# Optimization experiments

Hardware: AMD Instinct MI355X
Metric: run time of the kernel (lower is better)

Reference implementation:

```python
import jax, jax.numpy as jnp
import numpy as np

WORKSPACE_RADIUS = 1.0
WORKSPACE_HEIGHT = 1.0


def setup_inputs() -> dict:
    key = jax.random.key(0)
    k1, k2 = jax.random.split(key)
    # (B, N, 6): xyz + normals, already padded to common length N
    pointclouds = jax.random.normal(k1, (32, 131072, 6), dtype=jnp.float32)
    # (B, 4, 4): homogeneous task transforms
    task_transform = jax.random.normal(k2, (32, 4, 4), dtype=jnp.float32)
    return {"pointclouds": pointclouds, "task_transform": task_transform}


def reference(pointclouds, task_transform):
    # Split xyz points and normals
    pts = pointclouds[..., :3]          # (B, N, 3)
    nrm = pointclouds[..., 3:]          # (B, N, 3)

    rot = task_transform[:, :3, :3]     # (B, 3, 3)
    trans = task_transform[:, :3, 3]    # (B, 3)

    # points @ rotation + translation (matches torch.matmul(points, rotation))
    p = jnp.einsum('bnd,bde->bne', pts, rot) + trans[:, None, :]

    # padded rows have all-zero normals
    non_padded = jnp.sum(nrm, axis=-1) != 0

    sq_dist = p[..., 0] ** 2 + p[..., 1] ** 2
    in_range = (sq_dist < WORKSPACE_RADIUS ** 2) & (p[..., 2] < WORKSPACE_HEIGHT)
    valid = in_range & non_padded      # (B, N)

    # Filter-and-repad: compact valid points to the front (stable = order
    # preserving, as in the torch boolean-index version), zero the tail.
    order = jnp.argsort(~valid, axis=1, stable=True)                 # (B, N)
    gathered = jnp.take_along_axis(pointclouds, order[..., None], axis=1)
    mask_sorted = jnp.take_along_axis(valid, order, axis=1)
    return gathered * mask_sorted[..., None].astype(pointclouds.dtype)
```

## Files before the change

kernel.cpp:

```cpp
#include <hip/hip_runtime.h>
#include <cstdint>

namespace {

constexpr int kB   = 32;
constexpr int kN   = 131072;
constexpr int kC   = 6;
constexpr int TPB  = 256;
constexpr int ROWS_PER_BLK = 512;
constexpr int BPB  = kN / ROWS_PER_BLK;
constexpr int NBLK = kB * BPB;
constexpr int WAVES = TPB / 64;

__device__ __forceinline__ int waveSum(int v) {
#pragma unroll
    for (int off = 32; off; off >>= 1) v += __shfl_xor(v, off, 64);
    return v;
}

__global__ __launch_bounds__(TPB) void k_count(const float* __restrict__ pc,
                                               const float* __restrict__ tt,
                                               uint64_t* __restrict__ masks,
                                               int* __restrict__ blkCnt) {
    const int blk  = blockIdx.x;
    const int b    = blk >> 8;
    const int tid  = threadIdx.x;
    const int lane = tid & 63;
    const int wv   = tid >> 6;

    const float* T = tt + b * 16;
    const float T0 = T[0], T1 = T[1], T2 = T[2],  T3  = T[3];
    const float T4 = T[4], T5 = T[5], T6 = T[6],  T7  = T[7];
    const float T8 = T[8], T9 = T[9], T10 = T[10], T11 = T[11];

    const float4* f4 = (const float4*)pc + (size_t)blk * (ROWS_PER_BLK * kC / 4);
    const float4 q0 = f4[3 * tid];
    const float4 q1 = f4[3 * tid + 1];
    const float4 q2 = f4[3 * tid + 2];

    const float ns0 = (q0.w + q1.x) + q1.y;
    const float px0 = q0.x * T0 + q0.y * T4 + q0.z * T8  + T3;
    const float py0 = q0.x * T1 + q0.y * T5 + q0.z * T9  + T7;
    const float pz0 = q0.x * T2 + q0.y * T6 + q0.z * T10 + T11;
    const bool v0 = (px0 * px0 + py0 * py0 < 1.0f) && (pz0 < 1.0f) && (ns0 != 0.0f);

    const float ns1 = (q2.y + q2.z) + q2.w;
    const float px1 = q1.z * T0 + q1.w * T4 + q2.x * T8  + T3;
    const float py1 = q1.z * T1 + q1.w * T5 + q2.x * T9  + T7;
    const float pz1 = q1.z * T2 + q1.w * T6 + q2.x * T10 + T11;
    const bool v1 = (px1 * px1 + py1 * py1 < 1.0f) && (pz1 < 1.0f) && (ns1 != 0.0f);

    const uint64_t m0 = __ballot(v0);
    const uint64_t m1 = __ballot(v1);

    __shared__ uint64_t sm[WAVES * 2];
    if (lane == 0) {
        sm[wv * 2]     = m0;
        sm[wv * 2 + 1] = m1;
        masks[(size_t)blk * 8 + wv * 2]     = m0;
        masks[(size_t)blk * 8 + wv * 2 + 1] = m1;
    }
    __syncthreads();
    if (wv == 0) {
        int v = (lane < 8) ? __popcll(sm[lane]) : 0;
        v = waveSum(v);
        if (lane == 0) blkCnt[blk] = v;
    }
}

__global__ __launch_bounds__(TPB) void k_scatter(const float* __restrict__ pc,
                                                 const uint64_t* __restrict__ masks,
                                                 const int* __restrict__ blkCnt,
                                                 float* __restrict__ out) {
    const int blk  = blockIdx.x;
    const int b    = blk >> 8;
    const int sub  = blk & (BPB - 1);
    const int tid  = threadIdx.x;
    const int lane = tid & 63;
    const int wv   = tid >> 6;

    __shared__ uint64_t sm[8];
    __shared__ int sRed[2 * WAVES];

    if (tid < 8) sm[tid] = masks[(size_t)blk * 8 + tid];

    const int c = blkCnt[b * BPB + tid];
    const int pw = waveSum((tid < sub) ? c : 0);
    const int tw = waveSum(c);
    if (lane == 0) { sRed[wv] = pw; sRed[WAVES + wv] = tw; }
    __syncthreads();
    const int blockBase = (sRed[0] + sRed[1]) + (sRed[2] + sRed[3]);
    const int total     = (sRed[4] + sRed[5]) + (sRed[6] + sRed[7]);

    const uint64_t m0 = sm[wv * 2], m1 = sm[wv * 2 + 1];
    int wb = 0;
#pragma unroll
    for (int w = 0; w < WAVES - 1; ++w)
        if (w < wv) wb += __popcll(sm[w * 2]) + __popcll(sm[w * 2 + 1]);

    const uint64_t low = (1ull << lane) - 1ull;
    const int beforeE = __popcll(m0 & low) + __popcll(m1 & low);
    const bool v0 = (m0 >> lane) & 1ull;
    const bool v1 = (m1 >> lane) & 1ull;

    const size_t batchF = (size_t)b * kN * kC;
    const int rowBlk = sub * ROWS_PER_BLK + wv * 128 + 2 * lane;
    const int vcnt0 = blockBase + wb + beforeE;
    const int vcnt1 = vcnt0 + (v0 ? 1 : 0);

    if (v0) {
        const float2* r = (const float2*)(pc + batchF + (size_t)rowBlk * kC);
        float2* o = (float2*)(out + batchF + (size_t)vcnt0 * kC);
        o[0] = r[0]; o[1] = r[1]; o[2] = r[2];
    }
    if (v1) {
        const float2* r = (const float2*)(pc + batchF + (size_t)(rowBlk + 1) * kC);
        float2* o = (float2*)(out + batchF + (size_t)vcnt1 * kC);
        o[0] = r[0]; o[1] = r[1]; o[2] = r[2];
    }

    const int tail = kN - total;
    const int len  = (tail + BPB - 1) >> 8;
    const int r0 = total + sub * len;
    const int r1 = min(r0 + len, kN);
    if (r0 < r1) {
        float* base = out + batchF;
        const int f0 = r0 * 6, f1 = r1 * 6;
        if (tid == 0) {
            const float2 zz = make_float2(0.0f, 0.0f);
            if (f0 & 3) *(float2*)(base + f0) = zz;
            if (f1 & 3) *(float2*)(base + (f1 & ~3)) = zz;
        }
        const int a4 = (f0 + 3) >> 2;
        const int b4 = f1 >> 2;
        float4* o4 = (float4*)base;
        const float4 z4 = make_float4(0.0f, 0.0f, 0.0f, 0.0f);
        for (int i = a4 + tid; i < b4; i += TPB) o4[i] = z4;
    }
}

}

extern "C" void kernel_launch(void* const* d_in, const int* in_sizes, int n_in,
                              void* d_out, int out_size, void* d_ws, size_t ws_size,
                              hipStream_t stream) {
    const float* pc = (const float*)d_in[0];
    const float* tt = (const float*)d_in[1];
    float* out = (float*)d_out;

    uint64_t* masks = (uint64_t*)d_ws;
    int* blkCnt     = (int*)((char*)d_ws + (size_t)NBLK * 8 * sizeof(uint64_t));

    k_count<<<NBLK, TPB, 0, stream>>>(pc, tt, masks, blkCnt);
    k_scatter<<<NBLK, TPB, 0, stream>>>(pc, masks, blkCnt, out);
}
```

Measured before the change: 38.95 us.

## Stage block-compacted rows in workspace and emit them with contiguous copies

The first kernel now loads each block's rows coalesced through shared memory, compacts the valid rows within the block, and writes them to a per-block staging buffer in the workspace. The second kernel only copies each block's contiguous valid prefix to its global offset and zero-fills the tail, replacing per-thread scattered reads from the input. This trades sparse, uncoalesced gathers for an extra write and read of the valid data through the workspace, which can add traffic when many points are valid. The old two-kernel path is kept as a fallback when the workspace is too small.

Result: faster. 37.49 us (-3.7%).

```diff
diff --git a/kernel.cpp b/kernel.cpp
--- a/kernel.cpp
+++ b/kernel.cpp
@@ -11,6 +11,7 @@
 constexpr int BPB  = kN / ROWS_PER_BLK;
 constexpr int NBLK = kB * BPB;
 constexpr int WAVES = TPB / 64;
+constexpr int F4_PER_BLK = ROWS_PER_BLK * kC / 4;
 
 __device__ __forceinline__ int waveSum(int v) {
 #pragma unroll
@@ -18,10 +19,11 @@
     return v;
 }
 
-__global__ __launch_bounds__(TPB) void k_count(const float* __restrict__ pc,
-                                               const float* __restrict__ tt,
-                                               uint64_t* __restrict__ masks,
-                                               int* __restrict__ blkCnt) {
+
+__global__ __launch_bounds__(TPB) void k_count_stage(const float* __restrict__ pc,
+                                                     const float* __restrict__ tt,
+                                                     float* __restrict__ staged,
+                                                     int* __restrict__ blkCnt) {
     const int blk  = blockIdx.x;
     const int b    = blk >> 8;
     const int tid  = threadIdx.x;
@@ -33,45 +35,61 @@
     const float T4 = T[4], T5 = T[5], T6 = T[6],  T7  = T[7];
     const float T8 = T[8], T9 = T[9], T10 = T[10], T11 = T[11];
 
-    const float4* f4 = (const float4*)pc + (size_t)blk * (ROWS_PER_BLK * kC / 4);
-    const float4 q0 = f4[3 * tid];
-    const float4 q1 = f4[3 * tid + 1];
-    const float4 q2 = f4[3 * tid + 2];
-
-    const float ns0 = (q0.w + q1.x) + q1.y;
-    const float px0 = q0.x * T0 + q0.y * T4 + q0.z * T8  + T3;
-    const float py0 = q0.x * T1 + q0.y * T5 + q0.z * T9  + T7;
-    const float pz0 = q0.x * T2 + q0.y * T6 + q0.z * T10 + T11;
+    const float4* f4 = (const float4*)pc + (size_t)blk * F4_PER_BLK;
+    const float4 qa = f4[tid];
+    const float4 qb = f4[tid + 256];
+    const float4 qc = f4[tid + 512];
+
+    __shared__ float4 sb[F4_PER_BLK];
+    sb[tid] = qa; sb[tid + 256] = qb; sb[tid + 512] = qc;
+    __syncthreads();
+
+    const float2* s2 = (const float2*)sb;
+    const float2 r0a = s2[6 * tid],     r0b = s2[6 * tid + 1], r0c = s2[6 * tid + 2];
+    const float2 r1a = s2[6 * tid + 3], r1b = s2[6 * tid + 4], r1c = s2[6 * tid + 5];
+
+    const float ns0 = (r0b.y + r0c.x) + r0c.y;
+    const float px0 = r0a.x * T0 + r0a.y * T4 + r0b.x * T8  + T3;
+    const float py0 = r0a.x * T1 + r0a.y * T5 + r0b.x * T9  + T7;
+    const float pz0 = r0a.x * T2 + r0a.y * T6 + r0b.x * T10 + T11;
     const bool v0 = (px0 * px0 + py0 * py0 < 1.0f) && (pz0 < 1.0f) && (ns0 != 0.0f);
 
-    const float ns1 = (q2.y + q2.z) + q2.w;
-    const float px1 = q1.z * T0 + q1.w * T4 + q2.x * T8  + T3;
-    const float py1 = q1.z * T1 + q1.w * T5 + q2.x * T9  + T7;
-    const float pz1 = q1.z * T2 + q1.w * T6 + q2.x * T10 + T11;
+    const float ns1 = (r1b.y + r1c.x) + r1c.y;
+    const float px1 = r1a.x * T0 + r1a.y * T4 + r1b.x * T8  + T3;
+    const float py1 = r1a.x * T1 + r1a.y * T5 + r1b.x * T9  + T7;
+    const float pz1 = r1a.x * T2 + r1a.y * T6 + r1b.x * T10 + T11;
     const bool v1 = (px1 * px1 + py1 * py1 < 1.0f) && (pz1 < 1.0f) && (ns1 != 0.0f);
 
     const uint64_t m0 = __ballot(v0);
     const uint64_t m1 = __ballot(v1);
 
     __shared__ uint64_t sm[WAVES * 2];
-    if (lane == 0) {
-        sm[wv * 2]     = m0;
-        sm[wv * 2 + 1] = m1;
-        masks[(size_t)blk * 8 + wv * 2]     = m0;
-        masks[(size_t)blk * 8 + wv * 2 + 1] = m1;
-    }
-    __syncthreads();
+    if (lane == 0) { sm[wv * 2] = m0; sm[wv * 2 + 1] = m1; }
+    __syncthreads();
+
     if (wv == 0) {
         int v = (lane < 8) ? __popcll(sm[lane]) : 0;
         v = waveSum(v);
         if (lane == 0) blkCnt[blk] = v;
     }
-}
-
-__global__ __launch_bounds__(TPB) void k_scatter(const float* __restrict__ pc,
-                                                 const uint64_t* __restrict__ masks,
-                                                 const int* __restrict__ blkCnt,
-                                                 float* __restrict__ out) {
+
+    int wb = 0;
+#pragma unroll
+    for (int w = 0; w < WAVES - 1; ++w)
+        if (w < wv) wb += __popcll(sm[w * 2]) + __popcll(sm[w * 2 + 1]);
+    const uint64_t low = (1ull << lane) - 1ull;
+    const int beforeE = __popcll(m0 & low) + __popcll(m1 & low);
+    const int rk0 = wb + beforeE;
+    const int rk1 = rk0 + (v0 ? 1 : 0);
+
+    float2* st = (float2*)(staged + (size_t)blk * (ROWS_PER_BLK * kC));
+    if (v0) { float2* o = st + rk0 * 3; o[0] = r0a; o[1] = r0b; o[2] = r0c; }
+    if (v1) { float2* o = st + rk1 * 3; o[0] = r1a; o[1] = r1b; o[2] = r1c; }
+}
+
+__global__ __launch_bounds__(TPB) void k_emit(const float* __restrict__ staged,
+                                              const int* __restrict__ blkCnt,
+                                              float* __restrict__ out) {
     const int blk  = blockIdx.x;
     const int b    = blk >> 8;
     const int sub  = blk & (BPB - 1);
@@ -79,10 +97,7 @@
     const int lane = tid & 63;
     const int wv   = tid >> 6;
 
-    __shared__ uint64_t sm[8];
     __shared__ int sRed[2 * WAVES];
-
-    if (tid < 8) sm[tid] = masks[(size_t)blk * 8 + tid];
 
     const int c = blkCnt[b * BPB + tid];
     const int pw = waveSum((tid < sub) ? c : 0);
@@ -91,33 +106,14 @@
     __syncthreads();
     const int blockBase = (sRed[0] + sRed[1]) + (sRed[2] + sRed[3]);
     const int total     = (sRed[4] + sRed[5]) + (sRed[6] + sRed[7]);
-
-    const uint64_t m0 = sm[wv * 2], m1 = sm[wv * 2 + 1];
-    int wb = 0;
-#pragma unroll
-    for (int w = 0; w < WAVES - 1; ++w)
-        if (w < wv) wb += __popcll(sm[w * 2]) + __popcll(sm[w * 2 + 1]);
-
-    const uint64_t low = (1ull << lane) - 1ull;
-    const int beforeE = __popcll(m0 & low) + __popcll(m1 & low);
-    const bool v0 = (m0 >> lane) & 1ull;
-    const bool v1 = (m1 >> lane) & 1ull;
+    const int myCnt     = blkCnt[blk];
 
     const size_t batchF = (size_t)b * kN * kC;
-    const int rowBlk = sub * ROWS_PER_BLK + wv * 128 + 2 * lane;
-    const int vcnt0 = blockBase + wb + beforeE;
-    const int vcnt1 = vcnt0 + (v0 ? 1 : 0);
-
-    if (v0) {
-        const float2* r = (const float2*)(pc + batchF + (size_t)rowBlk * kC);
-        float2* o = (float2*)(out + batchF + (size_t)vcnt0 * kC);
-        o[0] = r[0]; o[1] = r[1]; o[2] = r[2];
-    }
-    if (v1) {
-        const float2* r = (const float2*)(pc + batchF + (size_t)(rowBlk + 1) * kC);
-        float2* o = (float2*)(out + batchF + (size_t)vcnt1 * kC);
-        o[0] = r[0]; o[1] = r[1]; o[2] = r[2];
-    }
+
+    const float2* src = (const float2*)(staged + (size_t)blk * (ROWS_PER_BLK * kC));
+    float2* dst = (float2*)(out + batchF + (size_t)blockBase * kC);
+    const int nf2 = myCnt * 3;
+    for (int i = tid; i < nf2; i += TPB) dst[i] = src[i];
 
     const int tail = kN - total;
     const int len  = (tail + BPB - 1) >> 8;
@@ -139,6 +135,128 @@
     }
 }
 
+
+__global__ __launch_bounds__(TPB) void k_count(const float* __restrict__ pc,
+                                               const float* __restrict__ tt,
+                                               uint64_t* __restrict__ masks,
+                                               int* __restrict__ blkCnt) {
+    const int blk  = blockIdx.x;
+    const int b    = blk >> 8;
+    const int tid  = threadIdx.x;
+    const int lane = tid & 63;
+    const int wv   = tid >> 6;
+
+    const float* T = tt + b * 16;
+    const float T0 = T[0], T1 = T[1], T2 = T[2],  T3  = T[3];
+    const float T4 = T[4], T5 = T[5], T6 = T[6],  T7  = T[7];
+    const float T8 = T[8], T9 = T[9], T10 = T[10], T11 = T[11];
+
+    const float4* f4 = (const float4*)pc + (size_t)blk * F4_PER_BLK;
+    const float4 q0 = f4[3 * tid];
+    const float4 q1 = f4[3 * tid + 1];
+    const float4 q2 = f4[3 * tid + 2];
+
+    const float ns0 = (q0.w + q1.x) + q1.y;
+    const float px0 = q0.x * T0 + q0.y * T4 + q0.z * T8  + T3;
+    const float py0 = q0.x * T1 + q0.y * T5 + q0.z * T9  + T7;
+    const float pz0 = q0.x * T2 + q0.y * T6 + q0.z * T10 + T11;
+    const bool v0 = (px0 * px0 + py0 * py0 < 1.0f) && (pz0 < 1.0f) && (ns0 != 0.0f);
+
+    const float ns1 = (q2.y + q2.z) + q2.w;
+    const float px1 = q1.z * T0 + q1.w * T4 + q2.x * T8  + T3;
+    const float py1 = q1.z * T1 + q1.w * T5 + q2.x * T9  + T7;
+    const float pz1 = q1.z * T2 + q1.w * T6 + q2.x * T10 + T11;
+    const bool v1 = (px1 * px1 + py1 * py1 < 1.0f) && (pz1 < 1.0f) && (ns1 != 0.0f);
+
+    const uint64_t m0 = __ballot(v0);
+    const uint64_t m1 = __ballot(v1);
+
+    __shared__ uint64_t sm[WAVES * 2];
+    if (lane == 0) {
+        sm[wv * 2]     = m0;
+        sm[wv * 2 + 1] = m1;
+        masks[(size_t)blk * 8 + wv * 2]     = m0;
+        masks[(size_t)blk * 8 + wv * 2 + 1] = m1;
+    }
+    __syncthreads();
+    if (wv == 0) {
+        int v = (lane < 8) ? __popcll(sm[lane]) : 0;
+        v = waveSum(v);
+        if (lane == 0) blkCnt[blk] = v;
+    }
+}
+
+__global__ __launch_bounds__(TPB) void k_scatter(const float* __restrict__ pc,
+                                                 const uint64_t* __restrict__ masks,
+                                                 const int* __restrict__ blkCnt,
+                                                 float* __restrict__ out) {
+    const int blk  = blockIdx.x;
+    const int b    = blk >> 8;
+    const int sub  = blk & (BPB - 1);
+    const int tid  = threadIdx.x;
+    const int lane = tid & 63;
+    const int wv   = tid >> 6;
+
+    __shared__ uint64_t sm[8];
+    __shared__ int sRed[2 * WAVES];
+
+    if (tid < 8) sm[tid] = masks[(size_t)blk * 8 + tid];
+
+    const int c = blkCnt[b * BPB + tid];
+    const int pw = waveSum((tid < sub) ? c : 0);
+    const int tw = waveSum(c);
+    if (lane == 0) { sRed[wv] = pw; sRed[WAVES + wv] = tw; }
+    __syncthreads();
+    const int blockBase = (sRed[0] + sRed[1]) + (sRed[2] + sRed[3]);
+    const int total     = (sRed[4] + sRed[5]) + (sRed[6] + sRed[7]);
+
+    const uint64_t m0 = sm[wv * 2], m1 = sm[wv * 2 + 1];
+    int wb = 0;
+#pragma unroll
+    for (int w = 0; w < WAVES - 1; ++w)
+        if (w < wv) wb += __popcll(sm[w * 2]) + __popcll(sm[w * 2 + 1]);
+
+    const uint64_t low = (1ull << lane) - 1ull;
+    const int beforeE = __popcll(m0 & low) + __popcll(m1 & low);
+    const bool v0 = (m0 >> lane) & 1ull;
+    const bool v1 = (m1 >> lane) & 1ull;
+
+    const size_t batchF = (size_t)b * kN * kC;
+    const int rowBlk = sub * ROWS_PER_BLK + wv * 128 + 2 * lane;
+    const int vcnt0 = blockBase + wb + beforeE;
+    const int vcnt1 = vcnt0 + (v0 ? 1 : 0);
+
+    if (v0) {
+        const float2* r = (const float2*)(pc + batchF + (size_t)rowBlk * kC);
+        float2* o = (float2*)(out + batchF + (size_t)vcnt0 * kC);
+        o[0] = r[0]; o[1] = r[1]; o[2] = r[2];
+    }
+    if (v1) {
+        const float2* r = (const float2*)(pc + batchF + (size_t)(rowBlk + 1) * kC);
+        float2* o = (float2*)(out + batchF + (size_t)vcnt1 * kC);
+        o[0] = r[0]; o[1] = r[1]; o[2] = r[2];
+    }
+
+    const int tail = kN - total;
+    const int len  = (tail + BPB - 1) >> 8;
+    const int r0 = total + sub * len;
+    const int r1 = min(r0 + len, kN);
+    if (r0 < r1) {
+        float* base = out + batchF;
+        const int f0 = r0 * 6, f1 = r1 * 6;
+        if (tid == 0) {
+            const float2 zz = make_float2(0.0f, 0.0f);
+            if (f0 & 3) *(float2*)(base + f0) = zz;
+            if (f1 & 3) *(float2*)(base + (f1 & ~3)) = zz;
+        }
+        const int a4 = (f0 + 3) >> 2;
+        const int b4 = f1 >> 2;
+        float4* o4 = (float4*)base;
+        const float4 z4 = make_float4(0.0f, 0.0f, 0.0f, 0.0f);
+        for (int i = a4 + tid; i < b4; i += TPB) o4[i] = z4;
+    }
+}
+
 }
 
 extern "C" void kernel_launch(void* const* d_in, const int* in_sizes, int n_in,
@@ -148,9 +266,18 @@
     const float* tt = (const float*)d_in[1];
     float* out = (float*)d_out;
 
-    uint64_t* masks = (uint64_t*)d_ws;
-    int* blkCnt     = (int*)((char*)d_ws + (size_t)NBLK * 8 * sizeof(uint64_t));
-
-    k_count<<<NBLK, TPB, 0, stream>>>(pc, tt, masks, blkCnt);
-    k_scatter<<<NBLK, TPB, 0, stream>>>(pc, masks, blkCnt, out);
-}
+    const size_t stagedBytes = (size_t)NBLK * ROWS_PER_BLK * kC * sizeof(float);
+    const size_t cntBytes    = (size_t)NBLK * sizeof(int);
+
+    if (ws_size >= stagedBytes + cntBytes) {
+        float* staged = (float*)d_ws;
+        int* blkCnt   = (int*)((char*)d_ws + stagedBytes);
+        k_count_stage<<<NBLK, TPB, 0, stream>>>(pc, tt, staged, blkCnt);
+        k_emit<<<NBLK, TPB, 0, stream>>>(staged, blkCnt, out);
+    } else {
+        uint64_t* masks = (uint64_t*)d_ws;
+        int* blkCnt     = (int*)((char*)d_ws + (size_t)NBLK * 8 * sizeof(uint64_t));
+        k_count<<<NBLK, TPB, 0, stream>>>(pc, tt, masks, blkCnt);
+        k_scatter<<<NBLK, TPB, 0, stream>>>(pc, masks, blkCnt, out);
+    }
+}
```
